# Optimization experiments

Measured on AMD Instinct MI355X. Metric: run time of the kernel, lower is better.

## Reference

```python
import jax, jax.numpy as jnp
import numpy as np

N_NODES = 100000
N_EDGES = 1600000
D_IN = 128
D_HID = 128
D_OUT = 64
N_GRAPHS = 128


def setup_inputs() -> dict:
    key = jax.random.key(0)
    ks = jax.random.split(key, 8)
    x = jax.random.normal(ks[0], (N_NODES, D_IN), dtype=jnp.float32)
    edge_index = jax.random.randint(ks[1], (2, N_EDGES), 0, N_NODES, dtype=jnp.int64)
    batch = jnp.sort(jax.random.randint(ks[2], (N_NODES,), 0, N_GRAPHS, dtype=jnp.int64))
    def glorot(k, fi, fo):
        s = jnp.sqrt(6.0 / (fi + fo)).astype(jnp.float32)
        return jax.random.uniform(k, (fi, fo), jnp.float32, -1.0, 1.0) * s
    return {
        "x": x, "edge_index": edge_index, "batch": batch,
        "W1": glorot(ks[3], D_IN, D_HID), "b1": jnp.zeros((D_HID,), jnp.float32),
        "W2": glorot(ks[4], D_HID, D_HID), "b2": jnp.zeros((D_HID,), jnp.float32),
        "W3": glorot(ks[5], D_HID, D_HID), "b3": jnp.zeros((D_HID,), jnp.float32),
        "Wfc": glorot(ks[6], D_HID, D_OUT), "bfc": jnp.zeros((D_OUT,), jnp.float32),
    }


def _gcn_graph(edge_index, n_nodes):
    # add self-loops and compute symmetric normalization (PyG gcn_norm)
    loop = jnp.arange(n_nodes, dtype=edge_index.dtype)
    src = jnp.concatenate([edge_index[0], loop])
    dst = jnp.concatenate([edge_index[1], loop])
    deg = jax.ops.segment_sum(jnp.ones_like(dst, dtype=jnp.float32), dst,
                              num_segments=n_nodes)
    dinv = jnp.where(deg > 0, jax.lax.rsqrt(deg), 0.0)
    norm = dinv[src] * dinv[dst]  # [E + N]
    return src, dst, norm


def _gcn_conv(x, src, dst, norm, W, b, n_nodes):
    h = x @ W                                    # [N, F_out]
    msg = h[src] * norm[:, None]                 # gather + scale
    agg = jax.ops.segment_sum(msg, dst, num_segments=n_nodes)  # scatter-add
    return agg + b


def reference(x, edge_index, batch, W1, b1, W2, b2, W3, b3, Wfc, bfc):
    n = x.shape[0]
    src, dst, norm = _gcn_graph(edge_index, n)
    h = jax.nn.relu(_gcn_conv(x, src, dst, norm, W1, b1, n))
    h = jax.nn.relu(_gcn_conv(h, src, dst, norm, W2, b2, n))
    h = jax.nn.relu(_gcn_conv(h, src, dst, norm, W3, b3, n))
    # global mean pool over graphs in the batch
    sums = jax.ops.segment_sum(h, batch, num_segments=N_GRAPHS)
    cnts = jax.ops.segment_sum(jnp.ones((n,), jnp.float32), batch,
                               num_segments=N_GRAPHS)
    pooled = sums / jnp.maximum(cnts, 1.0)[:, None]   # [G, D_HID]
    return pooled @ Wfc + bfc                         # [G, D_OUT]
```

## Files before the change

kernel.cpp:

```cpp
#include <hip/hip_runtime.h>

#define NN 100000
#define NE 1600000
#define DF 128
#define DOUT 64
#define NG 128
#define NB 391
#define EPB 8192
#define NBLKA ((NE + EPB - 1) / EPB)
#define PCH 8
#define NAGB (NN / 16)

typedef short short8 __attribute__((ext_vector_type(8)));
typedef float floatx4 __attribute__((ext_vector_type(4)));
typedef float floatx2 __attribute__((ext_vector_type(2)));

__device__ __forceinline__ unsigned short f2bf(float f) {
    unsigned int b = __float_as_uint(f);
    unsigned int r = (b + 0x7fffu + ((b >> 16) & 1u)) >> 16;
    return (unsigned short)r;
}
__device__ __forceinline__ float bf2f_lo(unsigned int v) { return __uint_as_float(v << 16); }
__device__ __forceinline__ float bf2f_hi(unsigned int v) { return __uint_as_float(v & 0xffff0000u); }

__device__ __forceinline__ int phi(int p) {
    return (((p >> 6) << 2) + (p & 3)) * 16 + ((p >> 2) & 15);
}


__global__ __launch_bounds__(256) void k_init(const int* __restrict__ dst,
                                              int* __restrict__ hist,
                                              const int* __restrict__ batch,
                                              int* __restrict__ gstart,
                                              int* __restrict__ ticket,
                                              int* __restrict__ col,
                                              const float* __restrict__ b1,
                                              const float* __restrict__ b2,
                                              const float* __restrict__ b3,
                                              float* __restrict__ bp,
                                              const float* __restrict__ W1,
                                              const float* __restrict__ W2,
                                              const float* __restrict__ W3,
                                              unsigned short* __restrict__ O1,
                                              unsigned short* __restrict__ O2,
                                              unsigned short* __restrict__ O3) {
    __shared__ int lh[NB];
    int blk = blockIdx.x;
    int t = threadIdx.x;
    if (blk < NBLKA) {
        for (int i = t; i < NB; i += 256) lh[i] = 0;
        __syncthreads();
        int e0 = blk * EPB;
        int e1 = min(e0 + EPB, NE);
        for (int e = e0 + t; e < e1; e += 256) atomicAdd(&lh[dst[e] >> 8], 1);
        __syncthreads();
        for (int i = t; i < NB; i += 256) hist[blk * NB + i] = lh[i];
    } else if (blk == NBLKA) {
        int g = t;
        if (g > NG) return;
        int lo = 0, hi = NN;
        while (lo < hi) {
            int mid = (lo + hi) >> 1;
            if (batch[mid] < g) lo = mid + 1; else hi = mid;
        }
        gstart[g] = lo;
    } else if (blk == NBLKA + 1) {
        if (t == 0) *ticket = 0;
        if (t >= 8 && t < 16) col[NE + (t - 8)] = 0;
        if (t < 128) {
            int c = phi(t);
            bp[t] = b1[c];
            bp[128 + t] = b2[c];
            bp[256 + t] = b3[c];
        }
    } else {
        int bb = blk - (NBLKA + 2);
        const float* W = (bb >= 16) ? W3 : (bb >= 8) ? W2 : W1;
        unsigned short* O = (bb >= 16) ? O3 : (bb >= 8) ? O2 : O1;
        bool logical = (bb < 8);
        int idx = (bb & 7) * 256 + t;
        int l = idx & 63;
        int s = (idx >> 6) & 3;
        int tt = idx >> 8;
        int k0 = s * 32 + (l >> 4) * 8;
        int c = tt * 16 + (l & 15);
        unsigned short o[8];
#pragma unroll
        for (int j = 0; j < 8; j++) {
            int kk = logical ? (k0 + j) : phi(k0 + j);
            o[j] = f2bf(W[kk * DF + c]);
        }
        *(short8*)&O[idx * 8] = *(short8*)o;
    }
}


__global__ __launch_bounds__(512) void k_scan(int* __restrict__ hist,
                                              int* __restrict__ bhist,
                                              int* __restrict__ bbase,
                                              int* __restrict__ ticket) {
    __shared__ int sh[512];
    __shared__ int amLast;
    int b = blockIdx.x, t = threadIdx.x;
    int v = (t < NBLKA) ? hist[t * NB + b] : 0;
    sh[t] = v;
    __syncthreads();
    for (int off = 1; off < 512; off <<= 1) {
        int a = (t >= off) ? sh[t - off] : 0;
        __syncthreads();
        sh[t] += a;
        __syncthreads();
    }
    if (t < NBLKA) hist[t * NB + b] = sh[t] - v;
    if (t == 511) atomicExch(&bhist[b], sh[511]);
    __syncthreads();
    if (t == 0) {
        __threadfence();
        amLast = (atomicAdd(ticket, 1) == NB - 1) ? 1 : 0;
    }
    __syncthreads();
    if (amLast) {
        int v2 = (t < NB) ? atomicAdd(&bhist[t], 0) : 0;
        __syncthreads();
        sh[t] = v2;
        __syncthreads();
        for (int off = 1; off < 512; off <<= 1) {
            int a = (t >= off) ? sh[t - off] : 0;
            __syncthreads();
            sh[t] += a;
            __syncthreads();
        }
        if (t < NB) bbase[t] = sh[t] - v2;
        if (t == NB - 1) bbase[NB] = sh[t];
    }
}

__global__ __launch_bounds__(256) void k_pairs(const int* __restrict__ src,
                                               const int* __restrict__ dst,
                                               const int* __restrict__ hist,
                                               const int* __restrict__ bbase,
                                               int* __restrict__ ebuf) {
    __shared__ int lh[NB];
    __shared__ int lbase[NB];
    int t = threadIdx.x;
    for (int i = t; i < NB; i += 256) {
        lh[i] = 0;
        lbase[i] = bbase[i] + hist[blockIdx.x * NB + i];
    }
    __syncthreads();
    int e0 = blockIdx.x * EPB;
    int e1 = min(e0 + EPB, NE);
    for (int e = e0 + t; e < e1; e += 256) {
        int s = src[e], d = dst[e];
        int bk = d >> 8;
        int off = atomicAdd(&lh[bk], 1);
        ebuf[lbase[bk] + off] = (s << 8) | (d & 255);
    }
}

__global__ __launch_bounds__(256) void k_build(const int* __restrict__ ebuf,
                                               const int* __restrict__ bbase,
                                               int* __restrict__ rowptr,
                                               float* __restrict__ dinv,
                                               int* __restrict__ col) {
    __shared__ int deg[256];
    __shared__ int lst[256];
    int b = blockIdx.x, t = threadIdx.x;
    int node = (b << 8) + t;
    deg[t] = 0;
    __syncthreads();
    int e0 = bbase[b], e1 = bbase[b + 1];
    for (int e = e0 + t; e < e1; e += 256) atomicAdd(&deg[ebuf[e] & 255], 1);
    __syncthreads();
    int v = deg[t];
    lst[t] = v;
    __syncthreads();
    for (int off = 1; off < 256; off <<= 1) {
        int a = (t >= off) ? lst[t - off] : 0;
        __syncthreads();
        lst[t] += a;
        __syncthreads();
    }
    int mystart = e0 + lst[t] - v;
    if (node < NN) {
        rowptr[node] = mystart;
        dinv[node] = rsqrtf((float)(v + 1));
    }
    if (b == NB - 1 && t == 255) rowptr[NN] = e1;
    lst[t] = mystart;
    __syncthreads();
    for (int e = e0 + t; e < e1; e += 256) {
        int pk = ebuf[e];
        int p = atomicAdd(&lst[pk & 255], 1);
        col[p] = (pk >> 8) * DF;
    }
}


__device__ __forceinline__ void gemm_core(const short8* af,
                                          const unsigned short* __restrict__ Wb,
                                          const float* __restrict__ dinv,
                                          int lane, int lm, int orow,
                                          unsigned char* __restrict__ fs8) {
    float dv[4];
#pragma unroll
    for (int j = 0; j < 4; j++) dv[j] = (orow + j < NN) ? dinv[orow + j] : 0.f;

    float res[4][8];
#pragma unroll
    for (int tt = 0; tt < 8; tt++) {
        floatx4 acc = {0.f, 0.f, 0.f, 0.f};
        const unsigned short* wp = Wb + ((size_t)(tt * 4) * 64 + lane) * 8;
        acc = __builtin_amdgcn_mfma_f32_16x16x32_bf16(af[0], *(const short8*)(wp), acc, 0, 0, 0);
        acc = __builtin_amdgcn_mfma_f32_16x16x32_bf16(af[1], *(const short8*)(wp + 512), acc, 0, 0, 0);
        acc = __builtin_amdgcn_mfma_f32_16x16x32_bf16(af[2], *(const short8*)(wp + 1024), acc, 0, 0, 0);
        acc = __builtin_amdgcn_mfma_f32_16x16x32_bf16(af[3], *(const short8*)(wp + 1536), acc, 0, 0, 0);
#pragma unroll
        for (int j = 0; j < 4; j++) res[j][tt] = acc[j] * dv[j];
    }

#pragma unroll
    for (int g = 0; g < 2; g++) {
#pragma unroll
        for (int j = 0; j < 4; j++) {
            int r = orow + j;
            if (r >= NN) continue;
            unsigned int w8 = __builtin_amdgcn_cvt_pk_fp8_f32(res[j][g * 4 + 0], res[j][g * 4 + 1], 0, false);
            w8 = __builtin_amdgcn_cvt_pk_fp8_f32(res[j][g * 4 + 2], res[j][g * 4 + 3], w8, true);
            *(unsigned int*)&fs8[(size_t)r * DF + g * 64 + lm * 4] = w8;
        }
    }
}

__global__ __launch_bounds__(256) void k_gemm1(const float* __restrict__ X,
                                               const unsigned short* __restrict__ Wb,
                                               const float* __restrict__ dinv,
                                               unsigned char* __restrict__ fs8) {
    int t = threadIdx.x;
    int wave = t >> 6, l = t & 63;
    int r0 = blockIdx.x * 64 + wave * 16;
    int lm = l & 15, q = l >> 4;

    int arow = r0 + lm;
    if (arow >= NN) arow = NN - 1;
    const float* xrow = X + (size_t)arow * DF + q * 8;
    short8 af[4];
#pragma unroll
    for (int s = 0; s < 4; s++) {
        float4 f0 = *(const float4*)(xrow + s * 32);
        float4 f1 = *(const float4*)(xrow + s * 32 + 4);
        unsigned short o[8] = {f2bf(f0.x), f2bf(f0.y), f2bf(f0.z), f2bf(f0.w),
                               f2bf(f1.x), f2bf(f1.y), f2bf(f1.z), f2bf(f1.w)};
        af[s] = *(short8*)o;
    }
    gemm_core(af, Wb, dinv, l, lm, r0 + q * 4, fs8);
}

__global__ __launch_bounds__(256) void k_gemm(const unsigned short* __restrict__ X,
                                              const unsigned short* __restrict__ Wb,
                                              const float* __restrict__ dinv,
                                              unsigned char* __restrict__ fs8) {
    int t = threadIdx.x;
    int wave = t >> 6, l = t & 63;
    int r0 = blockIdx.x * 64 + wave * 16;
    int lm = l & 15, q = l >> 4;

    int arow = r0 + lm;
    if (arow >= NN) arow = NN - 1;
    const unsigned short* xrow = X + (size_t)arow * DF + q * 8;
    short8 af[4];
#pragma unroll
    for (int s = 0; s < 4; s++) af[s] = *(const short8*)(xrow + s * 32);
    gemm_core(af, Wb, dinv, l, lm, r0 + q * 4, fs8);
}

__device__ __forceinline__ void agg_node(const unsigned char* __restrict__ fsl,
                                         const int* __restrict__ colb,
                                         size_t selfoff, int e0, int e1,
                                         float dvn, const float* bias,
                                         float* o) {
    floatx2 acc0 = {0.f, 0.f}, acc1 = {0.f, 0.f}, acc2 = {0.f, 0.f}, acc3 = {0.f, 0.f};
    for (int base = e0; base < e1; base += 8) {
        const int* cp = colb + base;
        int cb[8];
#pragma unroll
        for (int k = 0; k < 8; k++) cb[k] = cp[k];
        uint2 vv[8];
#pragma unroll
        for (int k = 0; k < 8; k++) vv[k] = *(const uint2*)(fsl + cb[k]);
#pragma unroll
        for (int k = 0; k < 8; k++) {
            if (base + k < e1) {
                acc0 += __builtin_amdgcn_cvt_pk_f32_fp8(vv[k].x, false);
                acc1 += __builtin_amdgcn_cvt_pk_f32_fp8(vv[k].x, true);
                acc2 += __builtin_amdgcn_cvt_pk_f32_fp8(vv[k].y, false);
                acc3 += __builtin_amdgcn_cvt_pk_f32_fp8(vv[k].y, true);
            }
        }
    }
    uint2 sv = *(const uint2*)(fsl + selfoff);
    acc0 += __builtin_amdgcn_cvt_pk_f32_fp8(sv.x, false);
    acc1 += __builtin_amdgcn_cvt_pk_f32_fp8(sv.x, true);
    acc2 += __builtin_amdgcn_cvt_pk_f32_fp8(sv.y, false);
    acc3 += __builtin_amdgcn_cvt_pk_f32_fp8(sv.y, true);

    float a[8] = {acc0.x, acc0.y, acc1.x, acc1.y, acc2.x, acc2.y, acc3.x, acc3.y};
#pragma unroll
    for (int j = 0; j < 8; j++) o[j] = fmaxf(dvn * a[j] + bias[j], 0.f);
}

__global__ __launch_bounds__(256) void k_agg(const unsigned char* __restrict__ fs8,
                                             const int* __restrict__ colb,
                                             const int* __restrict__ rowptr,
                                             const float* __restrict__ dinv,
                                             const float* __restrict__ bp,
                                             unsigned short* __restrict__ out) {
    int w = (int)((blockIdx.x * (size_t)blockDim.x + threadIdx.x) >> 6);
    int lane = threadIdx.x & 63;
    int sub = lane >> 4;
    int fo = lane & 15;
    int foff = fo * 8;
    int n = w * 4 + sub;

    float4 bA = *(const float4*)&bp[foff];
    float4 bB = *(const float4*)&bp[foff + 4];
    float bias[8] = {bA.x, bA.y, bA.z, bA.w, bB.x, bB.y, bB.z, bB.w};
    float dvn = dinv[n];
    int e0 = rowptr[n], e1 = rowptr[n + 1];

    float o[8];
    agg_node(fs8 + foff, colb, (size_t)n * DF, e0, e1, dvn, bias, o);

    uint4 pk;
    pk.x = (unsigned int)f2bf(o[0]) | ((unsigned int)f2bf(o[1]) << 16);
    pk.y = (unsigned int)f2bf(o[2]) | ((unsigned int)f2bf(o[3]) << 16);
    pk.z = (unsigned int)f2bf(o[4]) | ((unsigned int)f2bf(o[5]) << 16);
    pk.w = (unsigned int)f2bf(o[6]) | ((unsigned int)f2bf(o[7]) << 16);
    *(uint4*)&out[(size_t)n * DF + foff] = pk;
}


__global__ __launch_bounds__(256) void k_poolA(const unsigned short* __restrict__ h,
                                               const int* __restrict__ gstart,
                                               float* __restrict__ part) {
    __shared__ float2 red[256];
    int g = blockIdx.x >> 3, c = blockIdx.x & 7;
    int s = gstart[g], e = gstart[g + 1];
    int len = e - s;
    int cs = s + (int)(((long long)len * c) >> 3);
    int ce = s + (int)(((long long)len * (c + 1)) >> 3);
    int t = threadIdx.x;
    int fp = t & 63;
    int rs = t >> 6;
    float2 acc = make_float2(0.f, 0.f);
    for (int n = cs + rs; n < ce; n += 4) {
        unsigned int v = *(const unsigned int*)&h[(size_t)n * DF + fp * 2];
        acc.x += bf2f_lo(v);
        acc.y += bf2f_hi(v);
    }
    red[t] = acc;
    __syncthreads();
    if (rs == 0) {
        float2 a0 = red[fp], a1 = red[fp + 64], a2 = red[fp + 128], a3 = red[fp + 192];
        float2 o;
        o.x = (a0.x + a1.x) + (a2.x + a3.x);
        o.y = (a0.y + a1.y) + (a2.y + a3.y);
        *(float2*)&part[(size_t)blockIdx.x * DF + fp * 2] = o;
    }
}

__global__ __launch_bounds__(128) void k_poolfc(const float* __restrict__ part,
                                                const int* __restrict__ gstart,
                                                const float* __restrict__ Wfc,
                                                const float* __restrict__ bfc,
                                                float* __restrict__ out) {
    __shared__ float pl[DF];
    int g = blockIdx.x;
    int f = threadIdx.x;
    float s = 0.f;
#pragma unroll
    for (int c = 0; c < PCH; c++) s += part[(size_t)(g * PCH + c) * DF + f];
    int cnt = gstart[g + 1] - gstart[g];
    pl[phi(f)] = s / (float)max(cnt, 1);
    __syncthreads();
    if (f < DOUT) {
        float acc = bfc[f];
        for (int k = 0; k < DF; k++) acc += pl[k] * Wfc[k * DOUT + f];
        out[g * DOUT + f] = acc;
    }
}


extern "C" void kernel_launch(void* const* d_in, const int* in_sizes, int n_in,
                              void* d_out, int out_size, void* d_ws, size_t ws_size,
                              hipStream_t stream) {
    const float* x     = (const float*)d_in[0];
    const int*   ei    = (const int*)d_in[1];
    const int*   batch = (const int*)d_in[2];
    const float* W1 = (const float*)d_in[3];
    const float* b1 = (const float*)d_in[4];
    const float* W2 = (const float*)d_in[5];
    const float* b2 = (const float*)d_in[6];
    const float* W3 = (const float*)d_in[7];
    const float* b3 = (const float*)d_in[8];
    const float* Wfc = (const float*)d_in[9];
    const float* bfc = (const float*)d_in[10];
    float* out = (float*)d_out;

    char* p = (char*)d_ws;
    unsigned short* ob = (unsigned short*)p;  p += (size_t)NN * DF * sizeof(short);
    unsigned char*  fs8 = (unsigned char*)p;  p += (size_t)NN * DF + 256;
    unsigned short* Wb1 = (unsigned short*)p; p += 16384 * sizeof(short);
    unsigned short* Wb2 = (unsigned short*)p; p += 16384 * sizeof(short);
    unsigned short* Wb3 = (unsigned short*)p; p += 16384 * sizeof(short);
    float* dinv = (float*)p;           p += (size_t)NN * sizeof(float);
    int* rowptr = (int*)p;             p += (size_t)(NN + 4) * sizeof(int);
    int* col    = (int*)p;             p += (size_t)(NE + 8) * sizeof(int);
    int* ebuf   = (int*)p;             p += (size_t)NE * sizeof(int);
    int* bhist  = (int*)p;             p += (size_t)(NB + 4) * sizeof(int);
    int* bbase  = (int*)p;             p += (size_t)(NB + 4) * sizeof(int);
    int* hist   = (int*)p;             p += (size_t)NBLKA * NB * sizeof(int);
    int* gstart = (int*)p;             p += (size_t)(NG + 4) * sizeof(int);
    int* ticket = (int*)p;             p += 4 * sizeof(int);
    float* bp   = (float*)p;           p += 384 * sizeof(float);
    float* part = (float*)p;           p += (size_t)NG * PCH * DF * sizeof(float);

    const int* e_src = ei;
    const int* e_dst = ei + NE;

    k_init<<<NBLKA + 26, 256, 0, stream>>>(e_dst, hist, batch, gstart, ticket, col,
                                           b1, b2, b3, bp,
                                           W1, W2, W3, Wb1, Wb2, Wb3);
    k_scan<<<NB, 512, 0, stream>>>(hist, bhist, bbase, ticket);
    k_pairs<<<NBLKA, 256, 0, stream>>>(e_src, e_dst, hist, bbase, ebuf);
    k_build<<<NB, 256, 0, stream>>>(ebuf, bbase, rowptr, dinv, col);

    int ggrid = (NN + 63) / 64;

    k_gemm1<<<ggrid, 256, 0, stream>>>(x, Wb1, dinv, fs8);
    k_agg<<<NAGB, 256, 0, stream>>>(fs8, col, rowptr, dinv, bp, ob);
    k_gemm<<<ggrid, 256, 0, stream>>>(ob, Wb2, dinv, fs8);
    k_agg<<<NAGB, 256, 0, stream>>>(fs8, col, rowptr, dinv, bp + 128, ob);
    k_gemm<<<ggrid, 256, 0, stream>>>(ob, Wb3, dinv, fs8);
    k_agg<<<NAGB, 256, 0, stream>>>(fs8, col, rowptr, dinv, bp + 256, ob);

    k_poolA<<<NG * PCH, 256, 0, stream>>>(ob, gstart, part);
    k_poolfc<<<NG, 128, 0, stream>>>(part, gstart, Wfc, bfc, out);
}
```

Before: 329.0 us.

## Sort nodes by degree for aggregation load balance and shrink edge partition blocks

Builds a per-node degree histogram in the CSR build, scans it across blocks, and produces a permutation that groups nodes of similar in-degree. The aggregation kernel then processes nodes in that order, so the four nodes sharing a wavefront have similar edge counts and lanes idle less. Separately, the edges-per-block constant drops from 8192 to 2048, giving more partition blocks, and the scan now handles two histogram columns per thread to fit. The cost is two extra small kernels, an extra indirection on every aggregation load, and less locality in output writes.

```diff
diff --git a/kernel.cpp b/kernel.cpp
--- a/kernel.cpp
+++ b/kernel.cpp
@@ -6,7 +6,7 @@
 #define DOUT 64
 #define NG 128
 #define NB 391
-#define EPB 8192
+#define EPB 2048
 #define NBLKA ((NE + EPB - 1) / EPB)
 #define PCH 8
 #define NAGB (NN / 16)
@@ -102,8 +102,10 @@
     __shared__ int sh[512];
     __shared__ int amLast;
     int b = blockIdx.x, t = threadIdx.x;
-    int v = (t < NBLKA) ? hist[t * NB + b] : 0;
-    sh[t] = v;
+    int c0 = 2 * t, c1 = 2 * t + 1;
+    int v0 = (c0 < NBLKA) ? hist[c0 * NB + b] : 0;
+    int v1 = (c1 < NBLKA) ? hist[c1 * NB + b] : 0;
+    sh[t] = v0 + v1;
     __syncthreads();
     for (int off = 1; off < 512; off <<= 1) {
         int a = (t >= off) ? sh[t - off] : 0;
@@ -111,7 +113,9 @@
         sh[t] += a;
         __syncthreads();
     }
-    if (t < NBLKA) hist[t * NB + b] = sh[t] - v;
+    int excl = sh[t] - (v0 + v1);
+    if (c0 < NBLKA) hist[c0 * NB + b] = excl;
+    if (c1 < NBLKA) hist[c1 * NB + b] = excl + v0;
     if (t == 511) atomicExch(&bhist[b], sh[511]);
     __syncthreads();
     if (t == 0) {
@@ -162,12 +166,16 @@
                                                const int* __restrict__ bbase,
                                                int* __restrict__ rowptr,
                                                float* __restrict__ dinv,
-                                               int* __restrict__ col) {
+                                               int* __restrict__ col,
+                                               unsigned char* __restrict__ deg8,
+                                               int* __restrict__ dh) {
     __shared__ int deg[256];
     __shared__ int lst[256];
+    __shared__ int dbin[64];
     int b = blockIdx.x, t = threadIdx.x;
     int node = (b << 8) + t;
     deg[t] = 0;
+    if (t < 64) dbin[t] = 0;
     __syncthreads();
     int e0 = bbase[b], e1 = bbase[b + 1];
     for (int e = e0 + t; e < e1; e += 256) atomicAdd(&deg[ebuf[e] & 255], 1);
@@ -182,9 +190,12 @@
         __syncthreads();
     }
     int mystart = e0 + lst[t] - v;
+    int d8 = min(v, 63);
     if (node < NN) {
         rowptr[node] = mystart;
         dinv[node] = rsqrtf((float)(v + 1));
+        deg8[node] = (unsigned char)d8;
+        atomicAdd(&dbin[d8], 1);
     }
     if (b == NB - 1 && t == 255) rowptr[NN] = e1;
     lst[t] = mystart;
@@ -193,6 +204,53 @@
         int pk = ebuf[e];
         int p = atomicAdd(&lst[pk & 255], 1);
         col[p] = (pk >> 8) * DF;
+    }
+    __syncthreads();
+    if (t < 64) dh[b * 64 + t] = dbin[t];
+}
+
+__global__ __launch_bounds__(512) void k_dscan(int* __restrict__ dh,
+                                               int* __restrict__ dtot) {
+    __shared__ int sh[512];
+    int bin = blockIdx.x, t = threadIdx.x;
+    int v = (t < NB) ? dh[t * 64 + bin] : 0;
+    sh[t] = v;
+    __syncthreads();
+    for (int off = 1; off < 512; off <<= 1) {
+        int a = (t >= off) ? sh[t - off] : 0;
+        __syncthreads();
+        sh[t] += a;
+        __syncthreads();
+    }
+    if (t < NB) dh[t * 64 + bin] = sh[t] - v;
+    if (t == 511) dtot[bin] = sh[511];
+}
+
+__global__ __launch_bounds__(256) void k_dperm(const unsigned char* __restrict__ deg8,
+                                               const int* __restrict__ dh,
+                                               const int* __restrict__ dtot,
+                                               int* __restrict__ perm) {
+    __shared__ int dbase[64];
+    __shared__ int dcnt[64];
+    int b = blockIdx.x, t = threadIdx.x;
+    if (t < 64) dbase[t] = dtot[t];
+    __syncthreads();
+    for (int off = 1; off < 64; off <<= 1) {
+        int a = (t >= off && t < 64) ? dbase[t - off] : 0;
+        __syncthreads();
+        if (t < 64) dbase[t] += a;
+        __syncthreads();
+    }
+    if (t < 64) {
+        dbase[t] -= dtot[t];
+        dcnt[t] = 0;
+    }
+    __syncthreads();
+    int node = b * 256 + t;
+    if (node < NN) {
+        int d8 = deg8[node];
+        int off = atomicAdd(&dcnt[d8], 1);
+        perm[dbase[d8] + dh[b * 64 + d8] + off] = node;
     }
 }
 
@@ -314,13 +372,14 @@
                                              const int* __restrict__ rowptr,
                                              const float* __restrict__ dinv,
                                              const float* __restrict__ bp,
+                                             const int* __restrict__ perm,
                                              unsigned short* __restrict__ out) {
     int w = (int)((blockIdx.x * (size_t)blockDim.x + threadIdx.x) >> 6);
     int lane = threadIdx.x & 63;
     int sub = lane >> 4;
     int fo = lane & 15;
     int foff = fo * 8;
-    int n = w * 4 + sub;
+    int n = perm[w * 4 + sub];
 
     float4 bA = *(const float4*)&bp[foff];
     float4 bB = *(const float4*)&bp[foff + 4];
@@ -423,6 +482,10 @@
     int* gstart = (int*)p;             p += (size_t)(NG + 4) * sizeof(int);
     int* ticket = (int*)p;             p += 4 * sizeof(int);
     float* bp   = (float*)p;           p += 384 * sizeof(float);
+    unsigned char* deg8 = (unsigned char*)p; p += (size_t)(NN + 64);
+    int* dh     = (int*)p;             p += (size_t)NB * 64 * sizeof(int);
+    int* dtot   = (int*)p;             p += 64 * sizeof(int);
+    int* perm   = (int*)p;             p += (size_t)NN * sizeof(int);
     float* part = (float*)p;           p += (size_t)NG * PCH * DF * sizeof(float);
 
     const int* e_src = ei;
@@ -433,16 +496,18 @@
                                            W1, W2, W3, Wb1, Wb2, Wb3);
     k_scan<<<NB, 512, 0, stream>>>(hist, bhist, bbase, ticket);
     k_pairs<<<NBLKA, 256, 0, stream>>>(e_src, e_dst, hist, bbase, ebuf);
-    k_build<<<NB, 256, 0, stream>>>(ebuf, bbase, rowptr, dinv, col);
+    k_build<<<NB, 256, 0, stream>>>(ebuf, bbase, rowptr, dinv, col, deg8, dh);
+    k_dscan<<<64, 512, 0, stream>>>(dh, dtot);
+    k_dperm<<<NB, 256, 0, stream>>>(deg8, dh, dtot, perm);
 
     int ggrid = (NN + 63) / 64;
 
     k_gemm1<<<ggrid, 256, 0, stream>>>(x, Wb1, dinv, fs8);
-    k_agg<<<NAGB, 256, 0, stream>>>(fs8, col, rowptr, dinv, bp, ob);
+    k_agg<<<NAGB, 256, 0, stream>>>(fs8, col, rowptr, dinv, bp, perm, ob);
     k_gemm<<<ggrid, 256, 0, stream>>>(ob, Wb2, dinv, fs8);
-    k_agg<<<NAGB, 256, 0, stream>>>(fs8, col, rowptr, dinv, bp + 128, ob);
+    k_agg<<<NAGB, 256, 0, stream>>>(fs8, col, rowptr, dinv, bp + 128, perm, ob);
     k_gemm<<<ggrid, 256, 0, stream>>>(ob, Wb3, dinv, fs8);
-    k_agg<<<NAGB, 256, 0, stream>>>(fs8, col, rowptr, dinv, bp + 256, ob);
+    k_agg<<<NAGB, 256, 0, stream>>>(fs8, col, rowptr, dinv, bp + 256, perm, ob);
 
     k_poolA<<<NG * PCH, 256, 0, stream>>>(ob, gstart, part);
     k_poolfc<<<NG, 128, 0, stream>>>(part, gstart, Wfc, bfc, out);
```

After: 351.3 us. 1.07x slower.
